# Kernel tuning notes

Measured on AMD Instinct MI355X. Metric: run time of the kernel, lower is better.

## Reference

```python
import jax, jax.numpy as jnp
import numpy as np

N_HEADS = 16
MASK_NEG = -1e32


def setup_inputs() -> dict:
    key = jax.random.key(0)
    k0, k1, k2, k3, k4 = jax.random.split(key, 5)
    B, S, D = 8, 1024, 1024
    return {
        "q": jax.random.normal(k0, (B, S, D), dtype=jnp.float32),
        "k": jax.random.normal(k1, (B, S, D), dtype=jnp.float32),
        "v1": jax.random.normal(k2, (B, S, D), dtype=jnp.float32),
        "v2": jax.random.normal(k3, (B, S, D), dtype=jnp.float32),
        "counter_attention_mask": jax.random.randint(k4, (B, S), 0, 2, dtype=jnp.int32),
    }


def reference(q, k, v1, v2, counter_attention_mask):
    B, S, D = q.shape
    H = N_HEADS
    dk = D // H

    def split_heads(x):
        return x.reshape(B, S, H, dk).transpose(0, 2, 1, 3)  # [B,H,S,dk]

    qh, kh, v1h, v2h = split_heads(q), split_heads(k), split_heads(v1), split_heads(v2)

    # scaled dot-product scores [B,H,S,S]
    scores = jnp.einsum("bhqd,bhkd->bhqk", qh, kh) / jnp.sqrt(jnp.float32(dk))

    # create_mask(input, 0): allowed only where key_idx < query_idx (strict causal)
    i = jnp.arange(S)[:, None]
    j = jnp.arange(S)[None, :]
    allowed = j < i  # [S,S]
    scores = jnp.where(allowed[None, None], scores, MASK_NEG)

    # first softmax
    p = jax.nn.softmax(scores, axis=-1)

    # counter-attention mask: zero out masked key columns (per batch, all heads/rows)
    cm = counter_attention_mask[:, None, None, :]  # [B,1,1,S]
    p = jnp.where(cm == 1, jnp.float32(0.0), p)

    # second softmax over the (partially zeroed) probabilities
    p = jax.nn.softmax(p, axis=-1)

    # zero the first query row (pad_zero concat in the original)
    p = p.at[:, :, 0, :].set(0.0)

    out1 = jnp.einsum("bhqk,bhkd->bhqd", p, v1h)
    out2 = jnp.einsum("bhqk,bhkd->bhqd", p, v2h)

    def merge_heads(x):
        return x.transpose(0, 2, 1, 3).reshape(B, S, D)

    return merge_heads(out1), merge_heads(out2)
```

## Files before the change

kernel.cpp:

```cpp
#include <hip/hip_runtime.h>
#include <hip/hip_bf16.h>

#define B_ 8
#define S_ 1024
#define D_ 1024
#define H_ 16
#define DK_ 64
#define BH_ (B_ * H_)

typedef float f32x4 __attribute__((ext_vector_type(4)));
typedef short s16x8 __attribute__((ext_vector_type(8)));
typedef short s16x4 __attribute__((ext_vector_type(4)));

#define EXP2F(x) __builtin_amdgcn_exp2f(x)
#define LOG2E 1.44269504088896f

static __device__ __forceinline__ short f2b(float f) {
  unsigned u = __builtin_bit_cast(unsigned, f);
  u = u + 0x7FFFu + ((u >> 16) & 1u);
  return (short)(u >> 16);
}
static __device__ __forceinline__ short f2bn(float f) {
  __hip_bfloat16 h = __float2bfloat16(f);
  return __builtin_bit_cast(short, h);
}

static __device__ __forceinline__ int slotf(int g, int e) {
  return (e < 4) ? (4 * g + e) : (16 + 4 * g + (e - 4));
}


__global__ __launch_bounds__(256) void prep_k(const float* __restrict__ k,
                                              short* __restrict__ kb) {
  const int bid = blockIdx.x;
  const int s0 = (bid & 63) * 16;
  const int b = bid >> 6;
  const int tid = threadIdx.x;
#pragma unroll
  for (int it = 0; it < 8; ++it) {
    int li = it * 256 + tid;
    int s = s0 + (li >> 7);
    int ch = li & 127;
    int h = ch >> 3;
    int dk0 = (ch & 7) * 8;
    const float* src = k + ((size_t)(b * S_ + s)) * D_ + ch * 8;
    s16x8 o;
#pragma unroll
    for (int e = 0; e < 8; ++e) o[e] = f2b(src[e]);
    *(s16x8*)(kb + ((size_t)((b * H_ + h) * S_ + s)) * DK_ + dk0) = o;
  }
}

__global__ __launch_bounds__(256) void prep_v(const float* __restrict__ v1,
                                              const float* __restrict__ v2,
                                              short* __restrict__ v1f,
                                              short* __restrict__ v2f,
                                              float* __restrict__ vs) {
  const int bid = blockIdx.x;
  const int sg = bid & 3;
  const int h = (bid >> 2) & 15;
  const int b = bid >> 6;
  const int tid = threadIdx.x;
  const int db = tid >> 6;
  const int lane = tid & 63;
  const int r = lane & 15;
  const int g = lane >> 4;
  const size_t inbase = (size_t)b * S_ * D_ + h * DK_ + db * 16 + r;
  float s1 = 0.f, s2 = 0.f;
#pragma unroll
  for (int it = 0; it < 8; ++it) {
    int jt = sg * 8 + it;
    int j0 = jt * 32;
    s16x8 o1, o2;
#pragma unroll
    for (int e = 0; e < 8; ++e) {
      int j = j0 + slotf(g, e);
      float a = v1[inbase + (size_t)j * D_];
      float c = v2[inbase + (size_t)j * D_];
      s1 += a;
      s2 += c;
      o1[e] = f2b(a);
      o2[e] = f2b(c);
    }
    size_t off = (((size_t)((b * H_ + h) * 32 + jt) * 4 + db) * 64 + lane) * 8;
    *(s16x8*)(v1f + off) = o1;
    *(s16x8*)(v2f + off) = o2;
  }
  s1 += __shfl_xor(s1, 16);
  s1 += __shfl_xor(s1, 32);
  s2 += __shfl_xor(s2, 16);
  s2 += __shfl_xor(s2, 32);
  if (g == 0) {
    int dd = db * 16 + r;
    atomicAdd(&vs[(size_t)b * D_ + h * DK_ + dd], s1);
    atomicAdd(&vs[(size_t)(B_ + b) * D_ + h * DK_ + dd], s2);
  }
}

__global__ __launch_bounds__(256, 3) void attn_series2(
    const float* __restrict__ q, const short* __restrict__ kb,
    const short* __restrict__ v1f, const short* __restrict__ v2f,
    const int* __restrict__ cm, const float* __restrict__ vs,
    float* __restrict__ out) {
  const int bid = blockIdx.x;
  const int xcd = bid & 7;
  const int idx = bid >> 3;
  const int seg = 15 - (idx & 15);
  const int bhgrp = idx >> 4;
  const int bh = bhgrp * 8 + xcd;
  const int b = bh >> 4, h = bh & 15;

  const int tid = threadIdx.x;
  const int wid = tid >> 6;
  const int lane = tid & 63;
  const int r = lane & 15;
  const int g = lane >> 4;

  const int qw = seg * 64 + wid * 16;
  const int iq = qw + r;
  const int njt = 2 * seg + 2;

  __shared__ __align__(16) char sbuf[2][12288];
  __shared__ unsigned cmw[32];
  {
    const int* cmb = cm + b * S_;
#pragma unroll
    for (int it = 0; it < 4; ++it) {
      unsigned long long m = __ballot(cmb[it * 256 + tid] == 1);
      if (lane == 0) {
        int w0 = it * 8 + wid * 2;
        cmw[w0] = (unsigned)m;
        cmw[w0 + 1] = (unsigned)(m >> 32);
      }
    }
  }

  const float qscale = 0.125f * LOG2E;
  s16x8 qf0, qf1;
  {
    const float* qp = q + ((size_t)(b * S_ + qw + r)) * D_ + h * DK_;
#pragma unroll
    for (int e = 0; e < 8; ++e) qf0[e] = f2bn(qp[8 * g + e] * qscale);
#pragma unroll
    for (int e = 0; e < 8; ++e) qf1[e] = f2bn(qp[32 + 8 * g + e] * qscale);
  }

  const short* kbh = kb + (size_t)bh * S_ * DK_;
  const short* v1bh = v1f + (size_t)bh * 32 * 2048;
  const short* v2bh = v2f + (size_t)bh * 32 * 2048;

  const int srow = tid >> 3;
  const int sch = tid & 7;

#define SLK(reg, jtv) reg = *(const s16x8*)(kbh + (size_t)(jtv)*2048 + tid * 8);
#define SLV(d1, d2, jtv)                                           \
  {                                                                \
    d1 = *(const s16x8*)(v1bh + (size_t)(jtv)*2048 + tid * 8);     \
    d2 = *(const s16x8*)(v2bh + (size_t)(jtv)*2048 + tid * 8);     \
  }
#define SWK(buf, reg) \
  *(s16x8*)((buf) + srow * 128 + ((sch ^ (srow & 7)) * 16)) = reg;
#define SWV(buf, d1, d2)                        \
  {                                             \
    *(s16x8*)((buf) + 4096 + tid * 16) = d1;    \
    *(s16x8*)((buf) + 8192 + tid * 16) = d2;    \
  }
#define KFRAG(sK, row, quad) \
  (*(const s16x8*)((sK) + (row)*128 + (((quad) ^ ((row)&7)) * 16)))

  f32x4 a11[4], a12[4], a21[4], a22[4];
#pragma unroll
  for (int d0 = 0; d0 < 4; ++d0) {
    a11[d0] = (f32x4){0.f, 0.f, 0.f, 0.f};
    a12[d0] = (f32x4){0.f, 0.f, 0.f, 0.f};
    a21[d0] = (f32x4){0.f, 0.f, 0.f, 0.f};
    a22[d0] = (f32x4){0.f, 0.f, 0.f, 0.f};
  }
  float Z1 = 0.f, T1 = 0.f, T2 = 0.f;

  {
    s16x8 rk, rv1, rv2;
    SLK(rk, 0);
    SLV(rv1, rv2, 0);
    SWK(sbuf[0], rk);
    SWV(sbuf[0], rv1, rv2);
    __syncthreads();
    for (int jt = 0; jt < njt; ++jt) {
      const int jb = jt * 32;
      const char* sB = sbuf[jt & 1];
      const bool pf = (jt + 1 < njt);
      s16x8 rk2, rv12, rv22;
      if (pf) {
        SLK(rk2, jt + 1);
        SLV(rv12, rv22, jt + 1);
      }
      if (jb < qw + 16) {
        s16x8 k00 = KFRAG(sB, r, g);
        s16x8 k01 = KFRAG(sB, r, 4 + g);
        s16x8 k10 = KFRAG(sB, 16 + r, g);
        s16x8 k11 = KFRAG(sB, 16 + r, 4 + g);
        f32x4 s0 = {0.f, 0.f, 0.f, 0.f}, s1 = {0.f, 0.f, 0.f, 0.f};
        s0 = __builtin_amdgcn_mfma_f32_16x16x32_bf16(k00, qf0, s0, 0, 0, 0);
        s0 = __builtin_amdgcn_mfma_f32_16x16x32_bf16(k01, qf1, s0, 0, 0, 0);
        s1 = __builtin_amdgcn_mfma_f32_16x16x32_bf16(k10, qf0, s1, 0, 0, 0);
        s1 = __builtin_amdgcn_mfma_f32_16x16x32_bf16(k11, qf1, s1, 0, 0, 0);
        const unsigned cw = cmw[jt];
        const bool cb = (jb + 32 > qw);
        float w1[8], w2[8];
#pragma unroll
        for (int s2 = 0; s2 < 2; ++s2) {
          f32x4 sv = s2 ? s1 : s0;
#pragma unroll
          for (int e = 0; e < 4; ++e) {
            int sl = s2 * 16 + 4 * g + e;
            int j = jb + sl;
            float pe = EXP2F(sv[e]);
            if (cb) pe = (j < iq) ? pe : 0.f;
            Z1 += pe;
            float pm = ((cw >> sl) & 1u) ? 0.f : pe;
            float pm2 = pm * pm;
            T1 += pm;
            T2 += pm2;
            int o = s2 * 4 + e;
            w1[o] = pm;
            w2[o] = pm2;
          }
        }
        s16x8 wa1, wa2;
#pragma unroll
        for (int e = 0; e < 8; ++e) {
          wa1[e] = f2bn(w1[e]);
          wa2[e] = f2bn(w2[e]);
        }
        s16x8 vb1[4], vb2[4];
#pragma unroll
        for (int db = 0; db < 4; ++db) {
          vb1[db] = *(const s16x8*)(sB + 4096 + (db * 64 + lane) * 16);
          vb2[db] = *(const s16x8*)(sB + 8192 + (db * 64 + lane) * 16);
        }
#pragma unroll
        for (int db = 0; db < 4; ++db) {
          a11[db] = __builtin_amdgcn_mfma_f32_16x16x32_bf16(wa1, vb1[db], a11[db], 0, 0, 0);
          a21[db] = __builtin_amdgcn_mfma_f32_16x16x32_bf16(wa1, vb2[db], a21[db], 0, 0, 0);
          a12[db] = __builtin_amdgcn_mfma_f32_16x16x32_bf16(wa2, vb1[db], a12[db], 0, 0, 0);
          a22[db] = __builtin_amdgcn_mfma_f32_16x16x32_bf16(wa2, vb2[db], a22[db], 0, 0, 0);
        }
      }
      if (pf) {
        SWK(sbuf[(jt + 1) & 1], rk2);
        SWV(sbuf[(jt + 1) & 1], rv12, rv22);
      }
      __syncthreads();
    }
  }
#undef SLK
#undef SLV
#undef SWK
#undef SWV
#undef KFRAG

  Z1 += __shfl_xor(Z1, 16);
  Z1 += __shfl_xor(Z1, 32);
  T1 += __shfl_xor(T1, 16);
  T1 += __shfl_xor(T1, 32);
  T2 += __shfl_xor(T2, 16);
  T2 += __shfl_xor(T2, 32);

  const float iz = (Z1 > 0.f) ? (1.f / Z1) : 0.f;
  const float f1 = iz;
  const float f2 = 0.5f * iz * iz;
  const float Z2 = (float)S_ + T1 * f1 + T2 * f2;
  const float izz = 1.f / Z2;
  const float g1v = f1 * izz;
  const float g2v = f2 * izz;
  const float gcv = izz;

  float* out1 = out;
  float* out2 = out + (size_t)B_ * S_ * D_;
  const float* vs1 = vs + (size_t)b * D_ + h * DK_;
  const float* vs2 = vs + (size_t)(B_ + b) * D_ + h * DK_;

#pragma unroll
  for (int e = 0; e < 4; ++e) {
    float gg1 = __shfl(g1v, 4 * g + e);
    float gg2 = __shfl(g2v, 4 * g + e);
    float ggc = __shfl(gcv, 4 * g + e);
    int io = qw + 4 * g + e;
    bool zero = (io == 0);
    size_t ro = ((size_t)(b * S_) + io) * D_ + h * DK_;
#pragma unroll
    for (int db = 0; db < 4; ++db) {
      int dd = db * 16 + r;
      float o1 = a11[db][e] * gg1 + a12[db][e] * gg2 + vs1[dd] * ggc;
      float o2 = a21[db][e] * gg1 + a22[db][e] * gg2 + vs2[dd] * ggc;
      out1[ro + dd] = zero ? 0.f : o1;
      out2[ro + dd] = zero ? 0.f : o2;
    }
  }
}


__global__ __launch_bounds__(256) void vsum_kernel(const float* __restrict__ v1,
                                                   const float* __restrict__ v2,
                                                   float* __restrict__ vs) {
  int bid = blockIdx.x;
  int sc = bid & 7, dc = (bid >> 3) & 3, b = bid >> 5;
  int d = dc * 256 + threadIdx.x;
  const float* p1 = v1 + ((size_t)b * S_ + sc * 128) * D_ + d;
  const float* p2 = v2 + ((size_t)b * S_ + sc * 128) * D_ + d;
  float s1 = 0.f, s2 = 0.f;
  for (int j = 0; j < 128; ++j) {
    s1 += p1[(size_t)j * D_];
    s2 += p2[(size_t)j * D_];
  }
  atomicAdd(&vs[b * D_ + d], s1);
  atomicAdd(&vs[B_ * D_ + b * D_ + d], s2);
}

__global__ __launch_bounds__(256) void dualattn_fallback(
    const float* __restrict__ q, const float* __restrict__ k,
    const float* __restrict__ v1, const float* __restrict__ v2,
    const int* __restrict__ cm, const float* __restrict__ vs,
    float* __restrict__ out) {
  const int bid = blockIdx.x;
  const int qt = bid & 15;
  const int h = (bid >> 4) & 15;
  const int b = bid >> 8;
  const int tid = threadIdx.x;
  const int wid = tid >> 6;
  const int lane = tid & 63;
  const int r = lane & 15;
  const int g = lane >> 4;
  const int qw = qt * 64 + wid * 16;
  const int iq = qw + r;

  __shared__ __align__(16) char kbuf[32 * 128];
  __shared__ __align__(16) char vtb1[64 * 64];
  __shared__ __align__(16) char vtb2[64 * 64];
  __shared__ unsigned cmw[32];

  {
    const int* cmb = cm + b * S_;
#pragma unroll
    for (int it = 0; it < 4; ++it) {
      int c = cmb[it * 256 + tid];
      unsigned long long m = __ballot(c == 1);
      if (lane == 0) {
        int w0 = (it * 256 + wid * 64) >> 5;
        cmw[w0] = (unsigned)m;
        cmw[w0 + 1] = (unsigned)(m >> 32);
      }
    }
  }

  s16x8 qf0, qf1;
  {
    const float* qp = q + ((size_t)(b * S_) + qw + r) * D_ + h * DK_;
#pragma unroll
    for (int e = 0; e < 8; ++e) qf0[e] = f2b(qp[8 * g + e] * 0.125f);
#pragma unroll
    for (int e = 0; e < 8; ++e) qf1[e] = f2b(qp[32 + 8 * g + e] * 0.125f);
  }

  const int njt = 2 * qt + 2;
  const float* kbase = k + (size_t)(b * S_) * D_ + h * DK_;
  const float* v1base = v1 + (size_t)(b * S_) * D_ + h * DK_;
  const float* v2base = v2 + (size_t)(b * S_) * D_ + h * DK_;
  const int srow = tid >> 3;
  const int sch = tid & 7;

  float m1 = -INFINITY, Z1 = 0.f;
  for (int jt = 0; jt < njt; ++jt) {
    const int jbase = jt * 32;
    __syncthreads();
    {
      const float* kr = kbase + (size_t)(jbase + srow) * D_ + sch * 8;
      s16x8 pk;
#pragma unroll
      for (int e = 0; e < 8; ++e) pk[e] = f2b(kr[e]);
      *(s16x8*)(kbuf + srow * 128 + ((sch ^ (srow & 7)) * 16)) = pk;
    }
    __syncthreads();
    if (jbase < qw + 16) {
#pragma unroll
      for (int sub = 0; sub < 2; ++sub) {
        const int jsb = jbase + sub * 16;
        if (jsb < qw + 16) {
          const int row = sub * 16 + r;
          s16x8 ka0 = *(const s16x8*)(kbuf + row * 128 + ((g ^ (row & 7)) * 16));
          s16x8 ka1 = *(const s16x8*)(kbuf + row * 128 + (((4 + g) ^ (row & 7)) * 16));
          f32x4 sv = {0.f, 0.f, 0.f, 0.f};
          sv = __builtin_amdgcn_mfma_f32_16x16x32_bf16(ka0, qf0, sv, 0, 0, 0);
          sv = __builtin_amdgcn_mfma_f32_16x16x32_bf16(ka1, qf1, sv, 0, 0, 0);
          float tm = m1;
#pragma unroll
          for (int e = 0; e < 4; ++e) {
            int j = jsb + 4 * g + e;
            if (j < iq) tm = fmaxf(tm, sv[e]);
          }
          if (tm > m1) { Z1 *= __expf(m1 - tm); m1 = tm; }
#pragma unroll
          for (int e = 0; e < 4; ++e) {
            int j = jsb + 4 * g + e;
            if (j < iq) Z1 += __expf(sv[e] - tm);
          }
        }
      }
    }
  }
#pragma unroll
  for (int off = 16; off < 64; off <<= 1) {
    float mo = __shfl_xor(m1, off);
    float zo = __shfl_xor(Z1, off);
    float mn = fmaxf(m1, mo);
    if (mn > -INFINITY) {
      Z1 = Z1 * __expf(m1 - mn) + zo * __expf(mo - mn);
      m1 = mn;
    }
  }
  float z1i;
  if (m1 > -INFINITY) { z1i = 1.f / Z1; }
  else { z1i = 0.f; m1 = 0.f; }

  f32x4 acc1[4], acc2[4];
#pragma unroll
  for (int d0 = 0; d0 < 4; ++d0) {
    acc1[d0] = (f32x4){0.f, 0.f, 0.f, 0.f};
    acc2[d0] = (f32x4){0.f, 0.f, 0.f, 0.f};
  }
  float wsum = 0.f;

  for (int jt = 0; jt < njt; ++jt) {
    const int jbase = jt * 32;
    __syncthreads();
    {
      const float* kr = kbase + (size_t)(jbase + srow) * D_ + sch * 8;
      s16x8 pk;
#pragma unroll
      for (int e = 0; e < 8; ++e) pk[e] = f2b(kr[e]);
      *(s16x8*)(kbuf + srow * 128 + ((sch ^ (srow & 7)) * 16)) = pk;
      const float* v1r = v1base + (size_t)(jbase + srow) * D_ + sch * 8;
      const float* v2r = v2base + (size_t)(jbase + srow) * D_ + sch * 8;
#pragma unroll
      for (int e = 0; e < 8; ++e) {
        int dd = sch * 8 + e;
        int off = dd * 64 + (((srow >> 2) ^ (dd & 7)) * 8) + (srow & 3) * 2;
        *(short*)(vtb1 + off) = f2b(v1r[e]);
        *(short*)(vtb2 + off) = f2b(v2r[e]);
      }
    }
    __syncthreads();
    if (jbase < qw + 16) {
      const unsigned cmword = cmw[jbase >> 5];
      float w[8];
#pragma unroll
      for (int sub = 0; sub < 2; ++sub) {
        const int jsb = jbase + sub * 16;
        if (jsb < qw + 16) {
          const int row = sub * 16 + r;
          s16x8 ka0 = *(const s16x8*)(kbuf + row * 128 + ((g ^ (row & 7)) * 16));
          s16x8 ka1 = *(const s16x8*)(kbuf + row * 128 + (((4 + g) ^ (row & 7)) * 16));
          f32x4 sv = {0.f, 0.f, 0.f, 0.f};
          sv = __builtin_amdgcn_mfma_f32_16x16x32_bf16(ka0, qf0, sv, 0, 0, 0);
          sv = __builtin_amdgcn_mfma_f32_16x16x32_bf16(ka1, qf1, sv, 0, 0, 0);
#pragma unroll
          for (int e = 0; e < 4; ++e) {
            int j = jsb + 4 * g + e;
            float x = 0.f;
            if (j < iq && !((cmword >> (j & 31)) & 1u)) {
              float p = __expf(sv[e] - m1) * z1i;
              x = __expf(p) - 1.f;
            }
            w[sub * 4 + e] = x;
            wsum += x;
          }
        } else {
#pragma unroll
          for (int e = 0; e < 4; ++e) w[sub * 4 + e] = 0.f;
        }
      }
      s16x8 wa;
#pragma unroll
      for (int e = 0; e < 8; ++e) wa[e] = f2b(w[e]);
#pragma unroll
      for (int db = 0; db < 4; ++db) {
        const int dd = db * 16 + r;
        const int off0 = dd * 64 + ((g ^ (dd & 7)) * 8);
        const int off1 = dd * 64 + (((4 + g) ^ (dd & 7)) * 8);
        s16x4 lo1 = *(const s16x4*)(vtb1 + off0);
        s16x4 hi1 = *(const s16x4*)(vtb1 + off1);
        s16x8 vb1 = __builtin_shufflevector(lo1, hi1, 0, 1, 2, 3, 4, 5, 6, 7);
        acc1[db] = __builtin_amdgcn_mfma_f32_16x16x32_bf16(wa, vb1, acc1[db], 0, 0, 0);
        s16x4 lo2 = *(const s16x4*)(vtb2 + off0);
        s16x4 hi2 = *(const s16x4*)(vtb2 + off1);
        s16x8 vb2 = __builtin_shufflevector(lo2, hi2, 0, 1, 2, 3, 4, 5, 6, 7);
        acc2[db] = __builtin_amdgcn_mfma_f32_16x16x32_bf16(wa, vb2, acc2[db], 0, 0, 0);
      }
    }
  }

  wsum += __shfl_xor(wsum, 16);
  wsum += __shfl_xor(wsum, 32);
  const float z2 = (float)S_ + wsum;

  float* out1 = out;
  float* out2 = out + (size_t)B_ * S_ * D_;
#pragma unroll
  for (int e = 0; e < 4; ++e) {
    float z2e = __shfl(z2, 4 * g + e);
    float inv = 1.f / z2e;
    int io = qw + 4 * g + e;
    bool zero = (io == 0);
    size_t ro = ((size_t)(b * S_) + io) * D_ + h * DK_;
#pragma unroll
    for (int db = 0; db < 4; ++db) {
      int dd = db * 16 + r;
      float c1 = vs[(size_t)b * D_ + h * DK_ + dd];
      float c2 = vs[(size_t)(B_ + b) * D_ + h * DK_ + dd];
      out1[ro + dd] = zero ? 0.f : (acc1[db][e] + c1) * inv;
      out2[ro + dd] = zero ? 0.f : (acc2[db][e] + c2) * inv;
    }
  }
}


extern "C" void kernel_launch(void* const* d_in, const int* in_sizes, int n_in,
                              void* d_out, int out_size, void* d_ws, size_t ws_size,
                              hipStream_t stream) {
  (void)in_sizes; (void)n_in; (void)out_size;
  const float* q = (const float*)d_in[0];
  const float* k = (const float*)d_in[1];
  const float* v1 = (const float*)d_in[2];
  const float* v2 = (const float*)d_in[3];
  const int* cm = (const int*)d_in[4];
  float* outp = (float*)d_out;

  const size_t VS_BYTES = 2 * B_ * D_ * sizeof(float);
  const size_t FRAG_SHORTS = (size_t)BH_ * S_ * DK_;
  const size_t FRAG_BYTES = FRAG_SHORTS * 2;
  const size_t NEED = VS_BYTES + 3 * FRAG_BYTES;

  float* vs = (float*)d_ws;
  (void)hipMemsetAsync(vs, 0, VS_BYTES, stream);

  if (ws_size >= NEED) {
    short* kb = (short*)((char*)d_ws + VS_BYTES);
    short* v1f = kb + FRAG_SHORTS;
    short* v2f = v1f + FRAG_SHORTS;
    prep_k<<<B_ * (S_ / 16), 256, 0, stream>>>(k, kb);
    prep_v<<<B_ * H_ * 4, 256, 0, stream>>>(v1, v2, v1f, v2f, vs);
    attn_series2<<<2048, 256, 0, stream>>>(q, kb, v1f, v2f, cm, vs, outp);
  } else {
    vsum_kernel<<<256, 256, 0, stream>>>(v1, v2, vs);
    dualattn_fallback<<<B_ * H_ * 16, 256, 0, stream>>>(q, k, v1, v2, cm, vs, outp);
  }
}
```

Before: 110.9 us.

## Convert attention kernel to persistent blocks with atomic task queue

Replaces the 2048-block grid with 768 persistent blocks that pull (segment, batch-head) tasks from a global atomic counter, handing out the longest causal segments first. The aim is better load balance across CUs for the triangular workload and less tail imbalance. In exchange, the old XCD-aware mapping of heads to chiplets is dropped, which may hurt L2 reuse of K/V. It also adds an atomic and extra barriers per task, and the counter lives in workspace that is zeroed with a memset.

```diff
diff --git a/kernel.cpp b/kernel.cpp
--- a/kernel.cpp
+++ b/kernel.cpp
@@ -7,6 +7,8 @@
 #define H_ 16
 #define DK_ 64
 #define BH_ (B_ * H_)
+#define NTASK 2048
+#define NPERS 768
 
 typedef float f32x4 __attribute__((ext_vector_type(4)));
 typedef short s16x8 __attribute__((ext_vector_type(8)));
@@ -97,57 +99,20 @@
   }
 }
 
-__global__ __launch_bounds__(256, 3) void attn_series2(
+__global__ __launch_bounds__(256, 3) void attn_series2p(
     const float* __restrict__ q, const short* __restrict__ kb,
     const short* __restrict__ v1f, const short* __restrict__ v2f,
     const int* __restrict__ cm, const float* __restrict__ vs,
-    float* __restrict__ out) {
-  const int bid = blockIdx.x;
-  const int xcd = bid & 7;
-  const int idx = bid >> 3;
-  const int seg = 15 - (idx & 15);
-  const int bhgrp = idx >> 4;
-  const int bh = bhgrp * 8 + xcd;
-  const int b = bh >> 4, h = bh & 15;
-
+    unsigned* __restrict__ counter, float* __restrict__ out) {
   const int tid = threadIdx.x;
   const int wid = tid >> 6;
   const int lane = tid & 63;
   const int r = lane & 15;
   const int g = lane >> 4;
 
-  const int qw = seg * 64 + wid * 16;
-  const int iq = qw + r;
-  const int njt = 2 * seg + 2;
-
   __shared__ __align__(16) char sbuf[2][12288];
   __shared__ unsigned cmw[32];
-  {
-    const int* cmb = cm + b * S_;
-#pragma unroll
-    for (int it = 0; it < 4; ++it) {
-      unsigned long long m = __ballot(cmb[it * 256 + tid] == 1);
-      if (lane == 0) {
-        int w0 = it * 8 + wid * 2;
-        cmw[w0] = (unsigned)m;
-        cmw[w0 + 1] = (unsigned)(m >> 32);
-      }
-    }
-  }
-
-  const float qscale = 0.125f * LOG2E;
-  s16x8 qf0, qf1;
-  {
-    const float* qp = q + ((size_t)(b * S_ + qw + r)) * D_ + h * DK_;
-#pragma unroll
-    for (int e = 0; e < 8; ++e) qf0[e] = f2bn(qp[8 * g + e] * qscale);
-#pragma unroll
-    for (int e = 0; e < 8; ++e) qf1[e] = f2bn(qp[32 + 8 * g + e] * qscale);
-  }
-
-  const short* kbh = kb + (size_t)bh * S_ * DK_;
-  const short* v1bh = v1f + (size_t)bh * 32 * 2048;
-  const short* v2bh = v2f + (size_t)bh * 32 * 2048;
+  __shared__ int taskS;
 
   const int srow = tid >> 3;
   const int sch = tid & 7;
@@ -168,89 +133,172 @@
 #define KFRAG(sK, row, quad) \
   (*(const s16x8*)((sK) + (row)*128 + (((quad) ^ ((row)&7)) * 16)))
 
-  f32x4 a11[4], a12[4], a21[4], a22[4];
-#pragma unroll
-  for (int d0 = 0; d0 < 4; ++d0) {
-    a11[d0] = (f32x4){0.f, 0.f, 0.f, 0.f};
-    a12[d0] = (f32x4){0.f, 0.f, 0.f, 0.f};
-    a21[d0] = (f32x4){0.f, 0.f, 0.f, 0.f};
-    a22[d0] = (f32x4){0.f, 0.f, 0.f, 0.f};
-  }
-  float Z1 = 0.f, T1 = 0.f, T2 = 0.f;
-
-  {
-    s16x8 rk, rv1, rv2;
-    SLK(rk, 0);
-    SLV(rv1, rv2, 0);
-    SWK(sbuf[0], rk);
-    SWV(sbuf[0], rv1, rv2);
+  float* out1 = out;
+  float* out2 = out + (size_t)B_ * S_ * D_;
+
+  for (;;) {
     __syncthreads();
-    for (int jt = 0; jt < njt; ++jt) {
-      const int jb = jt * 32;
-      const char* sB = sbuf[jt & 1];
-      const bool pf = (jt + 1 < njt);
-      s16x8 rk2, rv12, rv22;
-      if (pf) {
-        SLK(rk2, jt + 1);
-        SLV(rv12, rv22, jt + 1);
-      }
-      if (jb < qw + 16) {
-        s16x8 k00 = KFRAG(sB, r, g);
-        s16x8 k01 = KFRAG(sB, r, 4 + g);
-        s16x8 k10 = KFRAG(sB, 16 + r, g);
-        s16x8 k11 = KFRAG(sB, 16 + r, 4 + g);
-        f32x4 s0 = {0.f, 0.f, 0.f, 0.f}, s1 = {0.f, 0.f, 0.f, 0.f};
-        s0 = __builtin_amdgcn_mfma_f32_16x16x32_bf16(k00, qf0, s0, 0, 0, 0);
-        s0 = __builtin_amdgcn_mfma_f32_16x16x32_bf16(k01, qf1, s0, 0, 0, 0);
-        s1 = __builtin_amdgcn_mfma_f32_16x16x32_bf16(k10, qf0, s1, 0, 0, 0);
-        s1 = __builtin_amdgcn_mfma_f32_16x16x32_bf16(k11, qf1, s1, 0, 0, 0);
-        const unsigned cw = cmw[jt];
-        const bool cb = (jb + 32 > qw);
-        float w1[8], w2[8];
-#pragma unroll
-        for (int s2 = 0; s2 < 2; ++s2) {
-          f32x4 sv = s2 ? s1 : s0;
-#pragma unroll
-          for (int e = 0; e < 4; ++e) {
-            int sl = s2 * 16 + 4 * g + e;
-            int j = jb + sl;
-            float pe = EXP2F(sv[e]);
-            if (cb) pe = (j < iq) ? pe : 0.f;
-            Z1 += pe;
-            float pm = ((cw >> sl) & 1u) ? 0.f : pe;
-            float pm2 = pm * pm;
-            T1 += pm;
-            T2 += pm2;
-            int o = s2 * 4 + e;
-            w1[o] = pm;
-            w2[o] = pm2;
-          }
+    if (tid == 0) taskS = (int)atomicAdd(counter, 1u);
+    __syncthreads();
+    const int task = taskS;
+    if (task >= NTASK) break;
+
+    const int seg = 15 - (task >> 7);
+    const int bh = task & 127;
+    const int b = bh >> 4, h = bh & 15;
+
+    const int qw = seg * 64 + wid * 16;
+    const int iq = qw + r;
+    const int njt = 2 * seg + 2;
+
+    {
+      const int* cmb = cm + b * S_;
+#pragma unroll
+      for (int it = 0; it < 4; ++it) {
+        unsigned long long m = __ballot(cmb[it * 256 + tid] == 1);
+        if (lane == 0) {
+          int w0 = it * 8 + wid * 2;
+          cmw[w0] = (unsigned)m;
+          cmw[w0 + 1] = (unsigned)(m >> 32);
         }
-        s16x8 wa1, wa2;
-#pragma unroll
-        for (int e = 0; e < 8; ++e) {
-          wa1[e] = f2bn(w1[e]);
-          wa2[e] = f2bn(w2[e]);
+      }
+    }
+
+    const float qscale = 0.125f * LOG2E;
+    s16x8 qf0, qf1;
+    {
+      const float* qp = q + ((size_t)(b * S_ + qw + r)) * D_ + h * DK_;
+#pragma unroll
+      for (int e = 0; e < 8; ++e) qf0[e] = f2bn(qp[8 * g + e] * qscale);
+#pragma unroll
+      for (int e = 0; e < 8; ++e) qf1[e] = f2bn(qp[32 + 8 * g + e] * qscale);
+    }
+
+    const short* kbh = kb + (size_t)bh * S_ * DK_;
+    const short* v1bh = v1f + (size_t)bh * 32 * 2048;
+    const short* v2bh = v2f + (size_t)bh * 32 * 2048;
+
+    f32x4 a11[4], a12[4], a21[4], a22[4];
+#pragma unroll
+    for (int d0 = 0; d0 < 4; ++d0) {
+      a11[d0] = (f32x4){0.f, 0.f, 0.f, 0.f};
+      a12[d0] = (f32x4){0.f, 0.f, 0.f, 0.f};
+      a21[d0] = (f32x4){0.f, 0.f, 0.f, 0.f};
+      a22[d0] = (f32x4){0.f, 0.f, 0.f, 0.f};
+    }
+    float Z1 = 0.f, T1 = 0.f, T2 = 0.f;
+
+    {
+      s16x8 rk, rv1, rv2;
+      SLK(rk, 0);
+      SLV(rv1, rv2, 0);
+      SWK(sbuf[0], rk);
+      SWV(sbuf[0], rv1, rv2);
+      __syncthreads();
+      for (int jt = 0; jt < njt; ++jt) {
+        const int jb = jt * 32;
+        const char* sB = sbuf[jt & 1];
+        const bool pf = (jt + 1 < njt);
+        s16x8 rk2, rv12, rv22;
+        if (pf) {
+          SLK(rk2, jt + 1);
+          SLV(rv12, rv22, jt + 1);
         }
-        s16x8 vb1[4], vb2[4];
-#pragma unroll
-        for (int db = 0; db < 4; ++db) {
-          vb1[db] = *(const s16x8*)(sB + 4096 + (db * 64 + lane) * 16);
-          vb2[db] = *(const s16x8*)(sB + 8192 + (db * 64 + lane) * 16);
+        if (jb < qw + 16) {
+          s16x8 k00 = KFRAG(sB, r, g);
+          s16x8 k01 = KFRAG(sB, r, 4 + g);
+          s16x8 k10 = KFRAG(sB, 16 + r, g);
+          s16x8 k11 = KFRAG(sB, 16 + r, 4 + g);
+          f32x4 s0 = {0.f, 0.f, 0.f, 0.f}, s1 = {0.f, 0.f, 0.f, 0.f};
+          s0 = __builtin_amdgcn_mfma_f32_16x16x32_bf16(k00, qf0, s0, 0, 0, 0);
+          s0 = __builtin_amdgcn_mfma_f32_16x16x32_bf16(k01, qf1, s0, 0, 0, 0);
+          s1 = __builtin_amdgcn_mfma_f32_16x16x32_bf16(k10, qf0, s1, 0, 0, 0);
+          s1 = __builtin_amdgcn_mfma_f32_16x16x32_bf16(k11, qf1, s1, 0, 0, 0);
+          const unsigned cw = cmw[jt];
+          const bool cb = (jb + 32 > qw);
+          float w1[8], w2[8];
+#pragma unroll
+          for (int s2 = 0; s2 < 2; ++s2) {
+            f32x4 sv = s2 ? s1 : s0;
+#pragma unroll
+            for (int e = 0; e < 4; ++e) {
+              int sl = s2 * 16 + 4 * g + e;
+              int j = jb + sl;
+              float pe = EXP2F(sv[e]);
+              if (cb) pe = (j < iq) ? pe : 0.f;
+              Z1 += pe;
+              float pm = ((cw >> sl) & 1u) ? 0.f : pe;
+              float pm2 = pm * pm;
+              T1 += pm;
+              T2 += pm2;
+              int o = s2 * 4 + e;
+              w1[o] = pm;
+              w2[o] = pm2;
+            }
+          }
+          s16x8 wa1, wa2;
+#pragma unroll
+          for (int e = 0; e < 8; ++e) {
+            wa1[e] = f2bn(w1[e]);
+            wa2[e] = f2bn(w2[e]);
+          }
+          s16x8 vb1[4], vb2[4];
+#pragma unroll
+          for (int db = 0; db < 4; ++db) {
+            vb1[db] = *(const s16x8*)(sB + 4096 + (db * 64 + lane) * 16);
+            vb2[db] = *(const s16x8*)(sB + 8192 + (db * 64 + lane) * 16);
+          }
+#pragma unroll
+          for (int db = 0; db < 4; ++db) {
+            a11[db] = __builtin_amdgcn_mfma_f32_16x16x32_bf16(wa1, vb1[db], a11[db], 0, 0, 0);
+            a21[db] = __builtin_amdgcn_mfma_f32_16x16x32_bf16(wa1, vb2[db], a21[db], 0, 0, 0);
+            a12[db] = __builtin_amdgcn_mfma_f32_16x16x32_bf16(wa2, vb1[db], a12[db], 0, 0, 0);
+            a22[db] = __builtin_amdgcn_mfma_f32_16x16x32_bf16(wa2, vb2[db], a22[db], 0, 0, 0);
+          }
         }
-#pragma unroll
-        for (int db = 0; db < 4; ++db) {
-          a11[db] = __builtin_amdgcn_mfma_f32_16x16x32_bf16(wa1, vb1[db], a11[db], 0, 0, 0);
-          a21[db] = __builtin_amdgcn_mfma_f32_16x16x32_bf16(wa1, vb2[db], a21[db], 0, 0, 0);
-          a12[db] = __builtin_amdgcn_mfma_f32_16x16x32_bf16(wa2, vb1[db], a12[db], 0, 0, 0);
-          a22[db] = __builtin_amdgcn_mfma_f32_16x16x32_bf16(wa2, vb2[db], a22[db], 0, 0, 0);
+        if (pf) {
+          SWK(sbuf[(jt + 1) & 1], rk2);
+          SWV(sbuf[(jt + 1) & 1], rv12, rv22);
         }
-      }
-      if (pf) {
-        SWK(sbuf[(jt + 1) & 1], rk2);
-        SWV(sbuf[(jt + 1) & 1], rv12, rv22);
-      }
-      __syncthreads();
+        __syncthreads();
+      }
+    }
+
+    Z1 += __shfl_xor(Z1, 16);
+    Z1 += __shfl_xor(Z1, 32);
+    T1 += __shfl_xor(T1, 16);
+    T1 += __shfl_xor(T1, 32);
+    T2 += __shfl_xor(T2, 16);
+    T2 += __shfl_xor(T2, 32);
+
+    const float iz = (Z1 > 0.f) ? (1.f / Z1) : 0.f;
+    const float f1 = iz;
+    const float f2 = 0.5f * iz * iz;
+    const float Z2 = (float)S_ + T1 * f1 + T2 * f2;
+    const float izz = 1.f / Z2;
+    const float g1v = f1 * izz;
+    const float g2v = f2 * izz;
+    const float gcv = izz;
+
+    const float* vs1 = vs + (size_t)b * D_ + h * DK_;
+    const float* vs2 = vs + (size_t)(B_ + b) * D_ + h * DK_;
+
+#pragma unroll
+    for (int e = 0; e < 4; ++e) {
+      float gg1 = __shfl(g1v, 4 * g + e);
+      float gg2 = __shfl(g2v, 4 * g + e);
+      float ggc = __shfl(gcv, 4 * g + e);
+      int io = qw + 4 * g + e;
+      bool zero = (io == 0);
+      size_t ro = ((size_t)(b * S_) + io) * D_ + h * DK_;
+#pragma unroll
+      for (int db = 0; db < 4; ++db) {
+        int dd = db * 16 + r;
+        float o1 = a11[db][e] * gg1 + a12[db][e] * gg2 + vs1[dd] * ggc;
+        float o2 = a21[db][e] * gg1 + a22[db][e] * gg2 + vs2[dd] * ggc;
+        out1[ro + dd] = zero ? 0.f : o1;
+        out2[ro + dd] = zero ? 0.f : o2;
+      }
     }
   }
 #undef SLK
@@ -258,45 +306,6 @@
 #undef SWK
 #undef SWV
 #undef KFRAG
-
-  Z1 += __shfl_xor(Z1, 16);
-  Z1 += __shfl_xor(Z1, 32);
-  T1 += __shfl_xor(T1, 16);
-  T1 += __shfl_xor(T1, 32);
-  T2 += __shfl_xor(T2, 16);
-  T2 += __shfl_xor(T2, 32);
-
-  const float iz = (Z1 > 0.f) ? (1.f / Z1) : 0.f;
-  const float f1 = iz;
-  const float f2 = 0.5f * iz * iz;
-  const float Z2 = (float)S_ + T1 * f1 + T2 * f2;
-  const float izz = 1.f / Z2;
-  const float g1v = f1 * izz;
-  const float g2v = f2 * izz;
-  const float gcv = izz;
-
-  float* out1 = out;
-  float* out2 = out + (size_t)B_ * S_ * D_;
-  const float* vs1 = vs + (size_t)b * D_ + h * DK_;
-  const float* vs2 = vs + (size_t)(B_ + b) * D_ + h * DK_;
-
-#pragma unroll
-  for (int e = 0; e < 4; ++e) {
-    float gg1 = __shfl(g1v, 4 * g + e);
-    float gg2 = __shfl(g2v, 4 * g + e);
-    float ggc = __shfl(gcv, 4 * g + e);
-    int io = qw + 4 * g + e;
-    bool zero = (io == 0);
-    size_t ro = ((size_t)(b * S_) + io) * D_ + h * DK_;
-#pragma unroll
-    for (int db = 0; db < 4; ++db) {
-      int dd = db * 16 + r;
-      float o1 = a11[db][e] * gg1 + a12[db][e] * gg2 + vs1[dd] * ggc;
-      float o2 = a21[db][e] * gg1 + a22[db][e] * gg2 + vs2[dd] * ggc;
-      out1[ro + dd] = zero ? 0.f : o1;
-      out2[ro + dd] = zero ? 0.f : o2;
-    }
-  }
 }
 
 
@@ -536,20 +545,23 @@
   float* outp = (float*)d_out;
 
   const size_t VS_BYTES = 2 * B_ * D_ * sizeof(float);
+  const size_t CTR_BYTES = 256;
   const size_t FRAG_SHORTS = (size_t)BH_ * S_ * DK_;
   const size_t FRAG_BYTES = FRAG_SHORTS * 2;
-  const size_t NEED = VS_BYTES + 3 * FRAG_BYTES;
+  const size_t NEED = VS_BYTES + CTR_BYTES + 3 * FRAG_BYTES;
 
   float* vs = (float*)d_ws;
-  (void)hipMemsetAsync(vs, 0, VS_BYTES, stream);
+  (void)hipMemsetAsync(d_ws, 0, VS_BYTES + CTR_BYTES, stream);
 
   if (ws_size >= NEED) {
-    short* kb = (short*)((char*)d_ws + VS_BYTES);
+    unsigned* counter = (unsigned*)((char*)d_ws + VS_BYTES);
+    short* kb = (short*)((char*)d_ws + VS_BYTES + CTR_BYTES);
     short* v1f = kb + FRAG_SHORTS;
     short* v2f = v1f + FRAG_SHORTS;
     prep_k<<<B_ * (S_ / 16), 256, 0, stream>>>(k, kb);
     prep_v<<<B_ * H_ * 4, 256, 0, stream>>>(v1, v2, v1f, v2f, vs);
-    attn_series2<<<2048, 256, 0, stream>>>(q, kb, v1f, v2f, cm, vs, outp);
+    attn_series2p<<<NPERS, 256, 0, stream>>>(q, kb, v1f, v2f, cm, vs, counter,
+                                             outp);
   } else {
     vsum_kernel<<<256, 256, 0, stream>>>(v1, v2, vs);
     dualattn_fallback<<<B_ * H_ * 16, 256, 0, stream>>>(q, k, v1, v2, cm, vs, outp);
```

Measured after the change: 119.7 us. 1.08x slower.
